# Optimization experiments

Hardware: AMD Instinct MI355X
Metric: run time of the kernel (lower is better)

Reference implementation:

```python
import jax, jax.numpy as jnp
import numpy as np

B, S, D, H = 1, 4096, 1024, 16
HD = D // H  # 64

def _precompute_freqs_cis(dim, end, theta=10000.0):
    freqs = 1.0 / theta ** (jnp.arange(0, dim, 2, dtype=jnp.float32) / dim)
    t = jnp.arange(end, dtype=jnp.float32)
    freqs = jnp.outer(t, freqs)
    return jnp.cos(freqs), jnp.sin(freqs)

def setup_inputs() -> dict:
    key = jax.random.key(0)
    ks = jax.random.split(key, 5)
    cos, sin = _precompute_freqs_cis(HD, S)
    scale = 1.0 / np.sqrt(D)
    return {
        "hidden_states": jax.random.normal(ks[0], (B, S, D), dtype=jnp.float32),
        "cos": cos,
        "sin": sin,
        "attention_mask": jnp.ones((B, S), dtype=jnp.float32),
        "Wq": jax.random.normal(ks[1], (D, D), dtype=jnp.float32) * scale,
        "Wk": jax.random.normal(ks[2], (D, D), dtype=jnp.float32) * scale,
        "Wv": jax.random.normal(ks[3], (D, D), dtype=jnp.float32) * scale,
        "Wo": jax.random.normal(ks[4], (D, D), dtype=jnp.float32) * scale,
    }

def _rope(x, cos, sin):
    # x: [B,S,H,HD]; cos/sin: [S,HD//2] -> broadcast [1,S,1,HD//2]
    c = cos[None, :, None, :]
    s = sin[None, :, None, :]
    x1, x2 = jnp.split(x, 2, axis=-1)
    return jnp.concatenate([x1 * c - x2 * s, x2 * c + x1 * s], axis=-1)

def reference(hidden_states, cos, sin, attention_mask, Wq, Wk, Wv, Wo):
    b, s, d = hidden_states.shape
    h, hd = H, HD
    q = (hidden_states @ Wq.T).reshape(b, s, h, hd)
    k = (hidden_states @ Wk.T).reshape(b, s, h, hd)
    v = (hidden_states @ Wv.T).reshape(b, s, h, hd)
    q = _rope(q, cos, sin)
    k = _rope(k, cos, sin)
    scaling = hd ** (-0.5)
    # [B,H,S,S] scores (naive full-matrix attention, matching source)
    scores = jnp.einsum('bqhd,bkhd->bhqk', q, k) * scaling
    mask_add = (1.0 - attention_mask)[:, None, None, :] * (-10000.0)
    scores = scores + mask_add
    attn = jax.nn.softmax(scores.astype(jnp.float32), axis=-1).astype(q.dtype)
    out = jnp.einsum('bhqk,bkhd->bqhd', attn, v).reshape(b, s, d)
    return out @ Wo.T
```

## Files before the change

kernel.cpp:

```cpp
#include <hip/hip_runtime.h>
#include <stdint.h>

#define S_LEN   4096
#define D_MODEL 1024
#define N_HEADS 16
#define HEAD_DIM 64
#define LDP 72

typedef __attribute__((ext_vector_type(8))) short bf16x8;
typedef __attribute__((ext_vector_type(4))) float f32x4;
typedef __attribute__((ext_vector_type(4))) unsigned short u16x4;
typedef unsigned short ushort_t;

#define LOG2E 1.44269504088896340736f
#define FIX_MAX 20.0f

__device__ __forceinline__ ushort_t f2bf(float f) {
    union { float f; uint32_t u; } v; v.f = f;
    uint32_t u = v.u;
    return (ushort_t)((u + 0x7fffu + ((u >> 16) & 1u)) >> 16);
}
__device__ __forceinline__ ushort_t f2bf_fast(float f) {
    union { float f; uint32_t u; } v; v.f = f;
    return (ushort_t)((v.u + 0x8000u) >> 16);
}
__device__ __forceinline__ float ex2(float x) {
#if __has_builtin(__builtin_amdgcn_exp2f)
    return __builtin_amdgcn_exp2f(x);
#else
    return exp2f(x);
#endif
}
__device__ __forceinline__ bf16x8 cvt8(const float* __restrict__ p) {
    bf16x8 r;
#pragma unroll
    for (int j = 0; j < 8; j++) r[j] = (short)f2bf(p[j]);
    return r;
}
__device__ __forceinline__ void gl_lds16(const ushort_t* g, ushort_t* l) {
    __builtin_amdgcn_global_load_lds(
        (const __attribute__((address_space(1))) void*)g,
        (__attribute__((address_space(3))) void*)l,
        16, 0, 0);
}

__global__ __launch_bounds__(256)
void cvt_kernel(const float* __restrict__ in, ushort_t* __restrict__ out, int n8)
{
    int i = blockIdx.x * 256 + threadIdx.x;
    if (i >= n8) return;
    *(bf16x8*)(out + (size_t)i * 8) = cvt8(in + (size_t)i * 8);
}

__global__ __launch_bounds__(256)
void madd_kernel(const float* __restrict__ mask, float* __restrict__ maddArr)
{
    int i = blockIdx.x * 256 + threadIdx.x;
    if (i < S_LEN)
        maddArr[i] = fmaf(1.0f - mask[i], -10000.0f * LOG2E, -FIX_MAX);
}

template <int ASYNC>
__global__ __launch_bounds__(256)
void qkv_kernel(const float* __restrict__ Xf, const ushort_t* __restrict__ Xb,
                const float* __restrict__ Wqf, const float* __restrict__ Wkf, const float* __restrict__ Wvf,
                const ushort_t* __restrict__ Wqb, const ushort_t* __restrict__ Wkb, const ushort_t* __restrict__ Wvb,
                ushort_t* __restrict__ Qo, ushort_t* __restrict__ Ko, ushort_t* __restrict__ Vto,
                const float* __restrict__ cosF, const float* __restrict__ sinF)
{
    __shared__ __align__(16) ushort_t As[128 * 64];
    __shared__ __align__(16) ushort_t Bs[128 * 64];

    const int t     = threadIdx.x;
    const int mode  = blockIdx.x >> 3;
    const int mBase = blockIdx.y * 128;
    const int nBase = (blockIdx.x & 7) * 128;
    const int lane  = t & 63;
    const int wid   = t >> 6;
    const int quad  = lane >> 4;
    const int l15   = lane & 15;
    const int sw    = l15 & 7;
    const int wm    = (wid & 1) * 64;
    const int wn    = (wid >> 1) * 64;

    const float*    Wf = (mode == 0) ? Wqf : (mode == 1) ? Wkf : Wvf;
    const ushort_t* Wb = (mode == 0) ? Wqb : (mode == 1) ? Wkb : Wvb;

    f32x4 acc[4][4];
#pragma unroll
    for (int i = 0; i < 4; i++)
#pragma unroll
        for (int j = 0; j < 4; j++) acc[i][j] = (f32x4)(0.0f);

    for (int k0 = 0; k0 < D_MODEL; k0 += 64) {
#pragma unroll
        for (int i = 0; i < 4; i++) {
            int e   = (i * 256 + t) * 8;
            int row = e >> 6;
            int c   = ((e >> 3) & 7) ^ (row & 7);
            if (ASYNC) {
                gl_lds16(&Xb[(size_t)(mBase + row) * D_MODEL + k0 + c * 8], &As[e]);
                gl_lds16(&Wb[(size_t)(nBase + row) * D_MODEL + k0 + c * 8], &Bs[e]);
            } else {
                *(bf16x8*)(&As[e]) = cvt8(&Xf[(size_t)(mBase + row) * D_MODEL + k0 + c * 8]);
                *(bf16x8*)(&Bs[e]) = cvt8(&Wf[(size_t)(nBase + row) * D_MODEL + k0 + c * 8]);
            }
        }
        __syncthreads();
#pragma unroll
        for (int ks = 0; ks < 2; ks++) {
            bf16x8 a[4], b[4];
            const int cc = ((ks * 4 + quad) ^ sw) * 8;
#pragma unroll
            for (int mt = 0; mt < 4; mt++)
                a[mt] = *(const bf16x8*)(&As[((wm + mt * 16 + l15) << 6) + cc]);
#pragma unroll
            for (int nt = 0; nt < 4; nt++)
                b[nt] = *(const bf16x8*)(&Bs[((wn + nt * 16 + l15) << 6) + cc]);
#pragma unroll
            for (int mt = 0; mt < 4; mt++)
#pragma unroll
                for (int nt = 0; nt < 4; nt++)
                    acc[mt][nt] = __builtin_amdgcn_mfma_f32_16x16x32_bf16(a[mt], b[nt], acc[mt][nt], 0, 0, 0);
        }
        __syncthreads();
    }

    if (mode == 2) {
#pragma unroll
        for (int mt = 0; mt < 4; mt++) {
            int m0 = mBase + wm + mt * 16 + quad * 4;
#pragma unroll
            for (int nt = 0; nt < 4; nt++) {
                int n = nBase + wn + nt * 16 + l15;
                u16x4 pk;
#pragma unroll
                for (int r = 0; r < 4; r++) pk[r] = f2bf(acc[mt][nt][r]);
                *(u16x4*)(&Vto[(size_t)n * S_LEN + m0]) = pk;
            }
        }
    } else {
        ushort_t* outB = (mode == 0) ? Qo : Ko;
        const float sc = (mode == 0) ? (0.125f * LOG2E) : 1.0f;
        const int hcb = nBase + wn;
#pragma unroll
        for (int nt = 0; nt < 2; nt++) {
            int f = nt * 16 + l15;
#pragma unroll
            for (int mt = 0; mt < 4; mt++) {
                int m0 = mBase + wm + mt * 16 + quad * 4;
#pragma unroll
                for (int r = 0; r < 4; r++) {
                    int srow = m0 + r;
                    float c = cosF[srow * 32 + f];
                    float s = sinF[srow * 32 + f];
                    float x1 = acc[mt][nt][r];
                    float x2 = acc[mt][nt + 2][r];
                    outB[(size_t)srow * D_MODEL + hcb + f]      = f2bf((x1 * c - x2 * s) * sc);
                    outB[(size_t)srow * D_MODEL + hcb + 32 + f] = f2bf((x2 * c + x1 * s) * sc);
                }
            }
        }
    }
}

template <int ASYNC>
__global__ __launch_bounds__(256)
void oproj_kernel(const ushort_t* __restrict__ Ab,
                  const float* __restrict__ Wf, const ushort_t* __restrict__ Wb,
                  float* __restrict__ outF)
{
    __shared__ __align__(16) ushort_t As[64 * 64];
    __shared__ __align__(16) ushort_t Bs[128 * 64];

    const int t     = threadIdx.x;
    const int mBase = blockIdx.y * 64;
    const int nBase = blockIdx.x * 128;
    const int lane  = t & 63;
    const int wid   = t >> 6;
    const int quad  = lane >> 4;
    const int l15   = lane & 15;
    const int sw    = l15 & 7;
    const int wm    = (wid & 1) * 32;
    const int wn    = (wid >> 1) * 64;

    f32x4 acc[2][4];
#pragma unroll
    for (int i = 0; i < 2; i++)
#pragma unroll
        for (int j = 0; j < 4; j++) acc[i][j] = (f32x4)(0.0f);

    for (int k0 = 0; k0 < D_MODEL; k0 += 64) {
#pragma unroll
        for (int i = 0; i < 2; i++) {
            int e = (i * 256 + t) * 8;
            int row = e >> 6;
            int c = ((e >> 3) & 7) ^ (row & 7);
            gl_lds16(&Ab[(size_t)(mBase + row) * D_MODEL + k0 + c * 8], &As[e]);
        }
#pragma unroll
        for (int i = 0; i < 4; i++) {
            int e = (i * 256 + t) * 8;
            int row = e >> 6;
            int c = ((e >> 3) & 7) ^ (row & 7);
            if (ASYNC) gl_lds16(&Wb[(size_t)(nBase + row) * D_MODEL + k0 + c * 8], &Bs[e]);
            else       *(bf16x8*)(&Bs[e]) = cvt8(&Wf[(size_t)(nBase + row) * D_MODEL + k0 + c * 8]);
        }
        __syncthreads();
#pragma unroll
        for (int ks = 0; ks < 2; ks++) {
            bf16x8 a[2], b[4];
            const int cc = ((ks * 4 + quad) ^ sw) * 8;
#pragma unroll
            for (int mt = 0; mt < 2; mt++)
                a[mt] = *(const bf16x8*)(&As[((wm + mt * 16 + l15) << 6) + cc]);
#pragma unroll
            for (int nt = 0; nt < 4; nt++)
                b[nt] = *(const bf16x8*)(&Bs[((wn + nt * 16 + l15) << 6) + cc]);
#pragma unroll
            for (int mt = 0; mt < 2; mt++)
#pragma unroll
                for (int nt = 0; nt < 4; nt++)
                    acc[mt][nt] = __builtin_amdgcn_mfma_f32_16x16x32_bf16(a[mt], b[nt], acc[mt][nt], 0, 0, 0);
        }
        __syncthreads();
    }

#pragma unroll
    for (int mt = 0; mt < 2; mt++) {
        int m0 = mBase + wm + mt * 16 + quad * 4;
#pragma unroll
        for (int nt = 0; nt < 4; nt++) {
            int n = nBase + wn + nt * 16 + l15;
#pragma unroll
            for (int r = 0; r < 4; r++)
                outF[(size_t)(m0 + r) * D_MODEL + n] = acc[mt][nt][r];
        }
    }
}

__global__ __launch_bounds__(256)
void attn_kernel(const ushort_t* __restrict__ Q, const ushort_t* __restrict__ K,
                 const ushort_t* __restrict__ Vt, const float* __restrict__ maddArr,
                 ushort_t* __restrict__ out)
{
    __shared__ __align__(16) ushort_t Ks[64 * 64];
    __shared__ __align__(16) ushort_t Vs[64 * 64];
    __shared__ __align__(16) ushort_t Ps[64 * LDP];

    const int t    = threadIdx.x;
    const int h    = blockIdx.y;
    const int qt   = blockIdx.x;
    const int lane = t & 63;
    const int wid  = t >> 6;
    const int quad = lane >> 4;
    const int l15  = lane & 15;
    const int sw   = l15 & 7;
    const int wq   = wid * 16;

#pragma unroll
    for (int i = 0; i < 2; i++) {
        int e = (i * 256 + t) * 8;
        int row = e >> 6;
        int c = ((e >> 3) & 7) ^ (row & 7);
        gl_lds16(&Q[(size_t)(qt * 64 + row) * D_MODEL + h * HEAD_DIM + c * 8], &Ks[e]);
    }
    __syncthreads();
    bf16x8 aq[2];
#pragma unroll
    for (int ks = 0; ks < 2; ks++)
        aq[ks] = *(const bf16x8*)(&Ks[((wq + l15) << 6) + (((ks * 4 + quad) ^ sw) << 3)]);
    __syncthreads();

    bf16x8 ones;
#pragma unroll
    for (int j = 0; j < 8; j++) ones[j] = (short)0x3F80;

    const int e0 = t * 8,            e1 = (256 + t) * 8;
    const int r0 = e0 >> 6,          r1 = e1 >> 6;
    const int c0 = ((e0 >> 3) & 7) ^ (r0 & 7);
    const int c1 = ((e1 >> 3) & 7) ^ (r1 & 7);
    const ushort_t* kS0 = K  + (size_t)r0 * D_MODEL + h * HEAD_DIM + c0 * 8;
    const ushort_t* kS1 = K  + (size_t)r1 * D_MODEL + h * HEAD_DIM + c1 * 8;
    const ushort_t* vS0 = Vt + (size_t)(h * HEAD_DIM + r0) * S_LEN + c0 * 8;
    const ushort_t* vS1 = Vt + (size_t)(h * HEAD_DIM + r1) * S_LEN + c1 * 8;
    const float*    mP  = maddArr + l15;

    ushort_t*       psw = &Ps[(wq + quad * 4) * LDP + l15];
    const ushort_t* psr = &Ps[(wq + l15) * LDP];

    f32x4 o_acc[4];
    f32x4 l_frag = (f32x4)(0.0f);
#pragma unroll
    for (int nt = 0; nt < 4; nt++) o_acc[nt] = (f32x4)(0.0f);

    for (int kt = 0; kt < S_LEN / 64; kt++) {
        gl_lds16(kS0, &Ks[e0]);
        gl_lds16(kS1, &Ks[e1]);
        gl_lds16(vS0, &Vs[e0]);
        gl_lds16(vS1, &Vs[e1]);
        kS0 += 64 * D_MODEL; kS1 += 64 * D_MODEL; vS0 += 64; vS1 += 64;
        float ma0 = mP[0], ma1 = mP[16], ma2 = mP[32], ma3 = mP[48];
        mP += 64;
        __syncthreads();

        f32x4 sacc[4];
        sacc[0] = (f32x4)(ma0);
        sacc[1] = (f32x4)(ma1);
        sacc[2] = (f32x4)(ma2);
        sacc[3] = (f32x4)(ma3);
#pragma unroll
        for (int ks = 0; ks < 2; ks++) {
            bf16x8 bk[4];
            const int cc = ((ks * 4 + quad) ^ sw) * 8;
#pragma unroll
            for (int nt = 0; nt < 4; nt++)
                bk[nt] = *(const bf16x8*)(&Ks[((nt * 16 + l15) << 6) + cc]);
#pragma unroll
            for (int nt = 0; nt < 4; nt++)
                sacc[nt] = __builtin_amdgcn_mfma_f32_16x16x32_bf16(aq[ks], bk[nt], sacc[nt], 0, 0, 0);
        }

#pragma unroll
        for (int r = 0; r < 4; r++) {
            psw[r * LDP]      = f2bf_fast(ex2(fminf(sacc[0][r], 0.0f)));
            psw[r * LDP + 16] = f2bf_fast(ex2(fminf(sacc[1][r], 0.0f)));
            psw[r * LDP + 32] = f2bf_fast(ex2(fminf(sacc[2][r], 0.0f)));
            psw[r * LDP + 48] = f2bf_fast(ex2(fminf(sacc[3][r], 0.0f)));
        }

#pragma unroll
        for (int ks = 0; ks < 2; ks++) {
            bf16x8 ap, bv[4];
            ap = *(const bf16x8*)(&psr[ks * 32 + quad * 8]);
            const int cc = ((ks * 4 + quad) ^ sw) * 8;
#pragma unroll
            for (int nt = 0; nt < 4; nt++)
                bv[nt] = *(const bf16x8*)(&Vs[((nt * 16 + l15) << 6) + cc]);
#pragma unroll
            for (int nt = 0; nt < 4; nt++)
                o_acc[nt] = __builtin_amdgcn_mfma_f32_16x16x32_bf16(ap, bv[nt], o_acc[nt], 0, 0, 0);
            l_frag = __builtin_amdgcn_mfma_f32_16x16x32_bf16(ap, ones, l_frag, 0, 0, 0);
        }
        __syncthreads();
    }

    float linv[4];
#pragma unroll
    for (int r = 0; r < 4; r++) linv[r] = 1.0f / fmaxf(l_frag[r], 1e-30f);

#pragma unroll
    for (int r = 0; r < 4; r++) {
        int srow = qt * 64 + wq + quad * 4 + r;
#pragma unroll
        for (int nt = 0; nt < 4; nt++) {
            int col = h * HEAD_DIM + nt * 16 + l15;
            out[(size_t)srow * D_MODEL + col] = f2bf(o_acc[nt][r] * linv[r]);
        }
    }
}

extern "C" void kernel_launch(void* const* d_in, const int* in_sizes, int n_in,
                              void* d_out, int out_size, void* d_ws, size_t ws_size,
                              hipStream_t stream)
{
    (void)in_sizes; (void)n_in; (void)out_size;

    const float* X    = (const float*)d_in[0];
    const float* cosF = (const float*)d_in[1];
    const float* sinF = (const float*)d_in[2];
    const float* mask = (const float*)d_in[3];
    const float* Wq   = (const float*)d_in[4];
    const float* Wk   = (const float*)d_in[5];
    const float* Wv   = (const float*)d_in[6];
    const float* Wo   = (const float*)d_in[7];

    const size_t SD = (size_t)S_LEN * D_MODEL;
    const size_t WD = (size_t)D_MODEL * D_MODEL;
    ushort_t* ws  = (ushort_t*)d_ws;
    ushort_t* Qb  = ws;
    ushort_t* Kb  = ws + SD;
    ushort_t* Vtb = ws + 2 * SD;
    ushort_t* Ab  = ws + 3 * SD;
    float* outF   = (float*)d_out;
    float* maddArr = outF;

    dim3 gQKV(24, 32), gO(8, 64), gA(S_LEN / 64, N_HEADS), bb(256);
    const bool big = ws_size >= (size_t)40 * 1024 * 1024;

    madd_kernel<<<S_LEN / 256, 256, 0, stream>>>(mask, maddArr);

    if (big) {
        ushort_t* Xb  = Ab;
        ushort_t* Wqb = ws + 4 * SD;
        ushort_t* Wkb = Wqb + WD;
        ushort_t* Wvb = Wkb + WD;
        ushort_t* Wob = Wvb + WD;

        cvt_kernel<<<(int)(SD / 8 / 256), 256, 0, stream>>>(X,  Xb,  (int)(SD / 8));
        cvt_kernel<<<(int)(WD / 8 / 256), 256, 0, stream>>>(Wq, Wqb, (int)(WD / 8));
        cvt_kernel<<<(int)(WD / 8 / 256), 256, 0, stream>>>(Wk, Wkb, (int)(WD / 8));
        cvt_kernel<<<(int)(WD / 8 / 256), 256, 0, stream>>>(Wv, Wvb, (int)(WD / 8));
        cvt_kernel<<<(int)(WD / 8 / 256), 256, 0, stream>>>(Wo, Wob, (int)(WD / 8));

        qkv_kernel<1><<<gQKV, bb, 0, stream>>>(nullptr, Xb, nullptr, nullptr, nullptr,
                                               Wqb, Wkb, Wvb, Qb, Kb, Vtb, cosF, sinF);
        attn_kernel<<<gA, bb, 0, stream>>>(Qb, Kb, Vtb, maddArr, Ab);
        oproj_kernel<1><<<gO, bb, 0, stream>>>(Ab, nullptr, Wob, outF);
    } else {
        qkv_kernel<0><<<gQKV, bb, 0, stream>>>(X, nullptr, Wq, Wk, Wv,
                                               nullptr, nullptr, nullptr, Qb, Kb, Vtb, cosF, sinF);
        attn_kernel<<<gA, bb, 0, stream>>>(Qb, Kb, Vtb, maddArr, Ab);
        oproj_kernel<0><<<gO, bb, 0, stream>>>(Ab, Wo, nullptr, outF);
    }
}
```

Baseline: 303.2 us.

## Double-buffer K/V tiles, process 128 queries per attention block, fuse conversion launches

The attention kernel now handles 128 query rows per block, with each wave owning 32 rows, so every K/V tile loaded into LDS is reused by twice as many MFMAs. K/V tiles are double-buffered, with the next tile's async load issued before computing on the current one, which drops one barrier per iteration. Q fragments are read straight from global memory instead of being staged through LDS. The five conversion launches and the mask launch are merged into one kernel to cut launch overhead. In exchange, the grid halves to 512 blocks and register and LDS use rise, which may lower occupancy.

```diff
diff --git a/kernel.cpp b/kernel.cpp
--- a/kernel.cpp
+++ b/kernel.cpp
@@ -45,11 +45,27 @@
 }
 
 __global__ __launch_bounds__(256)
-void cvt_kernel(const float* __restrict__ in, ushort_t* __restrict__ out, int n8)
-{
-    int i = blockIdx.x * 256 + threadIdx.x;
-    if (i >= n8) return;
-    *(bf16x8*)(out + (size_t)i * 8) = cvt8(in + (size_t)i * 8);
+void cvtall_kernel(const float* __restrict__ X,  const float* __restrict__ Wq,
+                   const float* __restrict__ Wk, const float* __restrict__ Wv,
+                   const float* __restrict__ Wo, const float* __restrict__ mask,
+                   ushort_t* __restrict__ Xb,  ushort_t* __restrict__ Wqb,
+                   ushort_t* __restrict__ Wkb, ushort_t* __restrict__ Wvb,
+                   ushort_t* __restrict__ Wob, float* __restrict__ maddArr)
+{
+    int b = blockIdx.x;
+    if (b < 4096) {
+        const float* src; ushort_t* dst; size_t off;
+        if (b < 2048)      { src = X;  dst = Xb;  off = (size_t)b * 2048; }
+        else if (b < 2560) { src = Wq; dst = Wqb; off = (size_t)(b - 2048) * 2048; }
+        else if (b < 3072) { src = Wk; dst = Wkb; off = (size_t)(b - 2560) * 2048; }
+        else if (b < 3584) { src = Wv; dst = Wvb; off = (size_t)(b - 3072) * 2048; }
+        else               { src = Wo; dst = Wob; off = (size_t)(b - 3584) * 2048; }
+        size_t i = off + (size_t)threadIdx.x * 8;
+        *(bf16x8*)(dst + i) = cvt8(src + i);
+    } else {
+        int i = (b - 4096) * 256 + threadIdx.x;
+        maddArr[i] = fmaf(1.0f - mask[i], -10000.0f * LOG2E, -FIX_MAX);
+    }
 }
 
 __global__ __launch_bounds__(256)
@@ -244,9 +260,9 @@
                  const ushort_t* __restrict__ Vt, const float* __restrict__ maddArr,
                  ushort_t* __restrict__ out)
 {
-    __shared__ __align__(16) ushort_t Ks[64 * 64];
-    __shared__ __align__(16) ushort_t Vs[64 * 64];
-    __shared__ __align__(16) ushort_t Ps[64 * LDP];
+    __shared__ __align__(16) ushort_t Ks[2][64 * 64];
+    __shared__ __align__(16) ushort_t Vs[2][64 * 64];
+    __shared__ __align__(16) ushort_t Ps[128 * LDP];
 
     const int t    = threadIdx.x;
     const int h    = blockIdx.y;
@@ -256,28 +272,22 @@
     const int quad = lane >> 4;
     const int l15  = lane & 15;
     const int sw   = l15 & 7;
-    const int wq   = wid * 16;
-
-#pragma unroll
-    for (int i = 0; i < 2; i++) {
-        int e = (i * 256 + t) * 8;
-        int row = e >> 6;
-        int c = ((e >> 3) & 7) ^ (row & 7);
-        gl_lds16(&Q[(size_t)(qt * 64 + row) * D_MODEL + h * HEAD_DIM + c * 8], &Ks[e]);
-    }
-    __syncthreads();
-    bf16x8 aq[2];
-#pragma unroll
-    for (int ks = 0; ks < 2; ks++)
-        aq[ks] = *(const bf16x8*)(&Ks[((wq + l15) << 6) + (((ks * 4 + quad) ^ sw) << 3)]);
-    __syncthreads();
+    const int wq   = wid * 32;
+
+    bf16x8 aq[2][2];
+#pragma unroll
+    for (int mt = 0; mt < 2; mt++)
+#pragma unroll
+        for (int ks = 0; ks < 2; ks++)
+            aq[mt][ks] = *(const bf16x8*)(&Q[(size_t)(qt * 128 + wq + mt * 16 + l15) * D_MODEL
+                                            + h * HEAD_DIM + ks * 32 + quad * 8]);
 
     bf16x8 ones;
 #pragma unroll
     for (int j = 0; j < 8; j++) ones[j] = (short)0x3F80;
 
-    const int e0 = t * 8,            e1 = (256 + t) * 8;
-    const int r0 = e0 >> 6,          r1 = e1 >> 6;
+    const int e0 = t * 8,   e1 = (256 + t) * 8;
+    const int r0 = e0 >> 6, r1 = e1 >> 6;
     const int c0 = ((e0 >> 3) & 7) ^ (r0 & 7);
     const int c1 = ((e1 >> 3) & 7) ^ (r1 & 7);
     const ushort_t* kS0 = K  + (size_t)r0 * D_MODEL + h * HEAD_DIM + c0 * 8;
@@ -286,76 +296,101 @@
     const ushort_t* vS1 = Vt + (size_t)(h * HEAD_DIM + r1) * S_LEN + c1 * 8;
     const float*    mP  = maddArr + l15;
 
-    ushort_t*       psw = &Ps[(wq + quad * 4) * LDP + l15];
-    const ushort_t* psr = &Ps[(wq + l15) * LDP];
-
-    f32x4 o_acc[4];
-    f32x4 l_frag = (f32x4)(0.0f);
-#pragma unroll
-    for (int nt = 0; nt < 4; nt++) o_acc[nt] = (f32x4)(0.0f);
+    f32x4 o_acc[2][4];
+    f32x4 l_frag[2];
+#pragma unroll
+    for (int mt = 0; mt < 2; mt++) {
+        l_frag[mt] = (f32x4)(0.0f);
+#pragma unroll
+        for (int nt = 0; nt < 4; nt++) o_acc[mt][nt] = (f32x4)(0.0f);
+    }
+
+    gl_lds16(kS0, &Ks[0][e0]);
+    gl_lds16(kS1, &Ks[0][e1]);
+    gl_lds16(vS0, &Vs[0][e0]);
+    gl_lds16(vS1, &Vs[0][e1]);
+    kS0 += 64 * D_MODEL; kS1 += 64 * D_MODEL; vS0 += 64; vS1 += 64;
 
     for (int kt = 0; kt < S_LEN / 64; kt++) {
-        gl_lds16(kS0, &Ks[e0]);
-        gl_lds16(kS1, &Ks[e1]);
-        gl_lds16(vS0, &Vs[e0]);
-        gl_lds16(vS1, &Vs[e1]);
-        kS0 += 64 * D_MODEL; kS1 += 64 * D_MODEL; vS0 += 64; vS1 += 64;
+        const int cur = kt & 1, nxt = cur ^ 1;
+        __syncthreads();
+
         float ma0 = mP[0], ma1 = mP[16], ma2 = mP[32], ma3 = mP[48];
         mP += 64;
-        __syncthreads();
-
-        f32x4 sacc[4];
-        sacc[0] = (f32x4)(ma0);
-        sacc[1] = (f32x4)(ma1);
-        sacc[2] = (f32x4)(ma2);
-        sacc[3] = (f32x4)(ma3);
+
+        if (kt < S_LEN / 64 - 1) {
+            gl_lds16(kS0, &Ks[nxt][e0]);
+            gl_lds16(kS1, &Ks[nxt][e1]);
+            gl_lds16(vS0, &Vs[nxt][e0]);
+            gl_lds16(vS1, &Vs[nxt][e1]);
+        }
+        kS0 += 64 * D_MODEL; kS1 += 64 * D_MODEL; vS0 += 64; vS1 += 64;
+
+        f32x4 sacc[2][4];
+#pragma unroll
+        for (int mt = 0; mt < 2; mt++) {
+            sacc[mt][0] = (f32x4)(ma0);
+            sacc[mt][1] = (f32x4)(ma1);
+            sacc[mt][2] = (f32x4)(ma2);
+            sacc[mt][3] = (f32x4)(ma3);
+        }
 #pragma unroll
         for (int ks = 0; ks < 2; ks++) {
             bf16x8 bk[4];
             const int cc = ((ks * 4 + quad) ^ sw) * 8;
 #pragma unroll
             for (int nt = 0; nt < 4; nt++)
-                bk[nt] = *(const bf16x8*)(&Ks[((nt * 16 + l15) << 6) + cc]);
+                bk[nt] = *(const bf16x8*)(&Ks[cur][((nt * 16 + l15) << 6) + cc]);
+#pragma unroll
+            for (int mt = 0; mt < 2; mt++)
+#pragma unroll
+                for (int nt = 0; nt < 4; nt++)
+                    sacc[mt][nt] = __builtin_amdgcn_mfma_f32_16x16x32_bf16(aq[mt][ks], bk[nt], sacc[mt][nt], 0, 0, 0);
+        }
+
+#pragma unroll
+        for (int mt = 0; mt < 2; mt++) {
+            ushort_t* psw = &Ps[(wq + mt * 16 + quad * 4) * LDP + l15];
+#pragma unroll
+            for (int r = 0; r < 4; r++) {
+                psw[r * LDP]      = f2bf_fast(ex2(fminf(sacc[mt][0][r], 0.0f)));
+                psw[r * LDP + 16] = f2bf_fast(ex2(fminf(sacc[mt][1][r], 0.0f)));
+                psw[r * LDP + 32] = f2bf_fast(ex2(fminf(sacc[mt][2][r], 0.0f)));
+                psw[r * LDP + 48] = f2bf_fast(ex2(fminf(sacc[mt][3][r], 0.0f)));
+            }
+        }
+
+#pragma unroll
+        for (int ks = 0; ks < 2; ks++) {
+            bf16x8 ap[2], bv[4];
+#pragma unroll
+            for (int mt = 0; mt < 2; mt++)
+                ap[mt] = *(const bf16x8*)(&Ps[(wq + mt * 16 + l15) * LDP + ks * 32 + quad * 8]);
+            const int cc = ((ks * 4 + quad) ^ sw) * 8;
 #pragma unroll
             for (int nt = 0; nt < 4; nt++)
-                sacc[nt] = __builtin_amdgcn_mfma_f32_16x16x32_bf16(aq[ks], bk[nt], sacc[nt], 0, 0, 0);
-        }
-
+                bv[nt] = *(const bf16x8*)(&Vs[cur][((nt * 16 + l15) << 6) + cc]);
+#pragma unroll
+            for (int mt = 0; mt < 2; mt++) {
+#pragma unroll
+                for (int nt = 0; nt < 4; nt++)
+                    o_acc[mt][nt] = __builtin_amdgcn_mfma_f32_16x16x32_bf16(ap[mt], bv[nt], o_acc[mt][nt], 0, 0, 0);
+                l_frag[mt] = __builtin_amdgcn_mfma_f32_16x16x32_bf16(ap[mt], ones, l_frag[mt], 0, 0, 0);
+            }
+        }
+    }
+
+#pragma unroll
+    for (int mt = 0; mt < 2; mt++) {
 #pragma unroll
         for (int r = 0; r < 4; r++) {
-            psw[r * LDP]      = f2bf_fast(ex2(fminf(sacc[0][r], 0.0f)));
-            psw[r * LDP + 16] = f2bf_fast(ex2(fminf(sacc[1][r], 0.0f)));
-            psw[r * LDP + 32] = f2bf_fast(ex2(fminf(sacc[2][r], 0.0f)));
-            psw[r * LDP + 48] = f2bf_fast(ex2(fminf(sacc[3][r], 0.0f)));
-        }
-
-#pragma unroll
-        for (int ks = 0; ks < 2; ks++) {
-            bf16x8 ap, bv[4];
-            ap = *(const bf16x8*)(&psr[ks * 32 + quad * 8]);
-            const int cc = ((ks * 4 + quad) ^ sw) * 8;
-#pragma unroll
-            for (int nt = 0; nt < 4; nt++)
-                bv[nt] = *(const bf16x8*)(&Vs[((nt * 16 + l15) << 6) + cc]);
-#pragma unroll
-            for (int nt = 0; nt < 4; nt++)
-                o_acc[nt] = __builtin_amdgcn_mfma_f32_16x16x32_bf16(ap, bv[nt], o_acc[nt], 0, 0, 0);
-            l_frag = __builtin_amdgcn_mfma_f32_16x16x32_bf16(ap, ones, l_frag, 0, 0, 0);
-        }
-        __syncthreads();
-    }
-
-    float linv[4];
-#pragma unroll
-    for (int r = 0; r < 4; r++) linv[r] = 1.0f / fmaxf(l_frag[r], 1e-30f);
-
-#pragma unroll
-    for (int r = 0; r < 4; r++) {
-        int srow = qt * 64 + wq + quad * 4 + r;
-#pragma unroll
-        for (int nt = 0; nt < 4; nt++) {
-            int col = h * HEAD_DIM + nt * 16 + l15;
-            out[(size_t)srow * D_MODEL + col] = f2bf(o_acc[nt][r] * linv[r]);
+            float inv = 1.0f / fmaxf(l_frag[mt][r], 1e-30f);
+            int srow = qt * 128 + wq + mt * 16 + quad * 4 + r;
+#pragma unroll
+            for (int nt = 0; nt < 4; nt++) {
+                int col = h * HEAD_DIM + nt * 16 + l15;
+                out[(size_t)srow * D_MODEL + col] = f2bf(o_acc[mt][nt][r] * inv);
+            }
         }
     }
 }
@@ -385,10 +420,8 @@
     float* outF   = (float*)d_out;
     float* maddArr = outF;
 
-    dim3 gQKV(24, 32), gO(8, 64), gA(S_LEN / 64, N_HEADS), bb(256);
+    dim3 gQKV(24, 32), gO(8, 64), gA(S_LEN / 128, N_HEADS), bb(256);
     const bool big = ws_size >= (size_t)40 * 1024 * 1024;
-
-    madd_kernel<<<S_LEN / 256, 256, 0, stream>>>(mask, maddArr);
 
     if (big) {
         ushort_t* Xb  = Ab;
@@ -397,17 +430,14 @@
         ushort_t* Wvb = Wkb + WD;
         ushort_t* Wob = Wvb + WD;
 
-        cvt_kernel<<<(int)(SD / 8 / 256), 256, 0, stream>>>(X,  Xb,  (int)(SD / 8));
-        cvt_kernel<<<(int)(WD / 8 / 256), 256, 0, stream>>>(Wq, Wqb, (int)(WD / 8));
-        cvt_kernel<<<(int)(WD / 8 / 256), 256, 0, stream>>>(Wk, Wkb, (int)(WD / 8));
-        cvt_kernel<<<(int)(WD / 8 / 256), 256, 0, stream>>>(Wv, Wvb, (int)(WD / 8));
-        cvt_kernel<<<(int)(WD / 8 / 256), 256, 0, stream>>>(Wo, Wob, (int)(WD / 8));
-
+        cvtall_kernel<<<4112, 256, 0, stream>>>(X, Wq, Wk, Wv, Wo, mask,
+                                                Xb, Wqb, Wkb, Wvb, Wob, maddArr);
         qkv_kernel<1><<<gQKV, bb, 0, stream>>>(nullptr, Xb, nullptr, nullptr, nullptr,
                                                Wqb, Wkb, Wvb, Qb, Kb, Vtb, cosF, sinF);
         attn_kernel<<<gA, bb, 0, stream>>>(Qb, Kb, Vtb, maddArr, Ab);
         oproj_kernel<1><<<gO, bb, 0, stream>>>(Ab, nullptr, Wob, outF);
     } else {
+        madd_kernel<<<S_LEN / 256, 256, 0, stream>>>(mask, maddArr);
         qkv_kernel<0><<<gQKV, bb, 0, stream>>>(X, nullptr, Wq, Wk, Wv,
                                                nullptr, nullptr, nullptr, Qb, Kb, Vtb, cosF, sinF);
         attn_kernel<<<gA, bb, 0, stream>>>(Qb, Kb, Vtb, maddArr, Ab);
```

Result: faster. 286.8 us (-5.4%).
